# Kernel tuning notes

Measured on AMD Instinct MI355X. Metric: run time of the kernel, lower is better.

## Reference

```python
import jax, jax.numpy as jnp
import numpy as np

EPS = 1e-6
K_HOPS = 2  # SGConv K


def setup_inputs() -> dict:
    key = jax.random.key(0)
    k1, k2, k3, k4 = jax.random.split(key, 4)
    B, Kk, C, T = 32, 8, 64, 250
    E, H = 4096, 128
    x = jax.random.normal(k1, (B, Kk, C, T), dtype=jnp.float32)
    edge_index = jax.random.randint(k2, (2, E), 0, C, dtype=jnp.int64)
    edge_weights = jax.random.uniform(k3, (E,), dtype=jnp.float32)
    W = jax.random.normal(k4, (H, Kk * T), dtype=jnp.float32) * 0.02
    b = jnp.zeros((H,), dtype=jnp.float32)
    return {"x": x, "edge_index": edge_index, "edge_weights": edge_weights, "W": W, "b": b}


def reference(x, edge_index, edge_weights, W, b):
    B, Kk, C, T = x.shape
    N = C  # nodes
    x = x.reshape(B, N, Kk * T)  # (B, N, F)

    # clamp non-positive edge weights to epsilon (mirrors in-place .data clamp)
    w = jnp.where(edge_weights <= 0, EPS, edge_weights)

    # gcn_norm with self loops (fill value 1.0)
    src, dst = edge_index[0], edge_index[1]
    loop = jnp.arange(N, dtype=edge_index.dtype)
    src = jnp.concatenate([src, loop])
    dst = jnp.concatenate([dst, loop])
    w = jnp.concatenate([w, jnp.ones((N,), w.dtype)])
    deg = jnp.zeros((N,), w.dtype).at[dst].add(w)
    dinv = jnp.where(deg > 0, deg ** -0.5, jnp.zeros_like(deg))
    norm = dinv[src] * w * dinv[dst]  # (E+N,)

    # K hops of gather -> weight -> scatter-add aggregation
    for _ in range(K_HOPS):
        msg = x[:, src, :] * norm[None, :, None]        # (B, E+N, F)
        x = jnp.zeros_like(x).at[:, dst, :].add(msg)    # (B, N, F)

    # final linear: y = x @ W^T + b
    return jnp.einsum('bnf,hf->bnh', x, W) + b
```

## Files before the change

kernel.cpp:

```cpp
#include <hip/hip_runtime.h>
#include <hip/hip_bf16.h>

#define EPSW 1e-6f

typedef __attribute__((ext_vector_type(4))) float floatx4;
typedef __attribute__((ext_vector_type(4))) unsigned int uintx4;
typedef __attribute__((ext_vector_type(8))) short shortx8;

__device__ __forceinline__ unsigned short f2bf(float f) {
    unsigned int u = __float_as_uint(f);
    u = (u + 0x7fffu + ((u >> 16) & 1u)) >> 16;
    return (unsigned short)u;
}

__device__ __forceinline__ unsigned int pk2(float lo, float hi) {
    return (unsigned int)f2bf(lo) | ((unsigned int)f2bf(hi) << 16);
}

__device__ __forceinline__ uintx4 pk8(floatx4 a, floatx4 b) {
    uintx4 r;
    r.x = pk2(a.x, a.y); r.y = pk2(a.z, a.w);
    r.z = pk2(b.x, b.y); r.w = pk2(b.z, b.w);
    return r;
}

__global__ __launch_bounds__(256) void gemm_mt(
        const float* __restrict__ x,
        const float* __restrict__ W,
        const int* __restrict__ ei,
        const float* __restrict__ ew,
        float* __restrict__ zp,
        float* __restrict__ Mt) {
    __shared__ __align__(16) unsigned char smem[2][20480];
    const int bid = blockIdx.x;
    const int t   = threadIdx.x;

    if (bid >= 512) {
        const int bm = bid - 512;
        float* A    = (float*)smem;
        float* deg  = A + 4096;
        float* dinv = deg + 64;
        if (t < 64) deg[t] = 1.0f;
        for (int i = t; i < 4096; i += 256) A[i] = 0.0f;
        __syncthreads();
        const int* srcp = ei;
        const int* dstp = ei + 4096;
#pragma unroll
        for (int i = 0; i < 16; ++i) {
            const int e = i * 256 + t;
            float w = ew[e];
            w = (w <= 0.0f) ? EPSW : w;
            atomicAdd(&deg[dstp[e]], w);
        }
        __syncthreads();
        if (t < 64) dinv[t] = 1.0f / sqrtf(deg[t]);
        __syncthreads();
#pragma unroll
        for (int i = 0; i < 16; ++i) {
            const int e = i * 256 + t;
            float w = ew[e];
            w = (w <= 0.0f) ? EPSW : w;
            const int s = srcp[e], d = dstp[e];
            atomicAdd(&A[d * 64 + s], dinv[s] * w * dinv[d]);
        }
        if (t < 64) atomicAdd(&A[t * 64 + t], dinv[t] * dinv[t]);
        __syncthreads();
        const int c  = t & 63;
        const int rr = t >> 6;
        float s0 = 0.f, s1 = 0.f, s2 = 0.f, s3 = 0.f;
#pragma unroll 8
        for (int k = 0; k < 64; ++k) {
            const float akc = A[k * 64 + c];
            const float* an = A + (bm * 16 + rr * 4) * 64 + k;
            s0 += an[0]   * akc;
            s1 += an[64]  * akc;
            s2 += an[128] * akc;
            s3 += an[192] * akc;
        }
        float* mo = Mt + c * 64 + bm * 16 + rr * 4;
        mo[0] = s0; mo[1] = s1; mo[2] = s2; mo[3] = s3;
        return;
    }

    const int ks    = bid & 7;
    const int bb2   = bid >> 3;
    const int rbase = bb2 * 32;
    const int kbase = ks * 256;

    const int wave = t >> 6, lane = t & 63;
    const int m = lane & 15, q = lane >> 4;
    const int kq = t & 7;
    const int rw = t >> 3;

    floatx4 acc[2][2];
#pragma unroll
    for (int rt = 0; rt < 2; ++rt)
#pragma unroll
        for (int hh = 0; hh < 2; ++hh)
            acc[rt][hh] = (floatx4){0.f, 0.f, 0.f, 0.f};

    floatx4 rA[2][2];
    floatx4 rB[2][8];

#define LOADC(c)                                                              \
    {                                                                         \
        const int s_ = (c) & 1;                                               \
        const int k_ = kbase + (c) * 64 + kq * 8;                             \
        if (k_ < 2000) {                                                      \
            const float* pa_ = x + (size_t)(rbase + rw) * 2000 + k_;          \
            rA[s_][0] = *(const floatx4*)pa_;                                 \
            rA[s_][1] = *(const floatx4*)(pa_ + 4);                           \
            _Pragma("unroll")                                                 \
            for (int j_ = 0; j_ < 4; ++j_) {                                  \
                const float* pw_ = W + (size_t)(rw + 32 * j_) * 2000 + k_;    \
                rB[s_][j_ * 2]     = *(const floatx4*)pw_;                    \
                rB[s_][j_ * 2 + 1] = *(const floatx4*)(pw_ + 4);              \
            }                                                                 \
        } else {                                                              \
            rA[s_][0] = rA[s_][1] = (floatx4){0.f, 0.f, 0.f, 0.f};            \
            _Pragma("unroll")                                                 \
            for (int j_ = 0; j_ < 8; ++j_)                                    \
                rB[s_][j_] = (floatx4){0.f, 0.f, 0.f, 0.f};                   \
        }                                                                     \
    }

#define WRITEC(c)                                                             \
    {                                                                         \
        const int s_ = (c) & 1;                                               \
        unsigned char* sb_ = smem[s_];                                        \
        *(uintx4*)(sb_ + kq * 512 + rw * 16) = pk8(rA[s_][0], rA[s_][1]);     \
        _Pragma("unroll")                                                     \
        for (int j_ = 0; j_ < 4; ++j_)                                        \
            *(uintx4*)(sb_ + 4096 + kq * 2048 + (rw + 32 * j_) * 16) =        \
                pk8(rB[s_][j_ * 2], rB[s_][j_ * 2 + 1]);                      \
    }

    LOADC(0);
    LOADC(1);
#pragma unroll
    for (int c = 0; c < 4; ++c) {
        WRITEC(c);
        if (c < 2) LOADC(c + 2);
        __syncthreads();
        const unsigned char* sb = smem[c & 1];
#pragma unroll
        for (int p = 0; p < 2; ++p) {
            const int kgq = p * 4 + q;
            shortx8 af[2];
#pragma unroll
            for (int rt = 0; rt < 2; ++rt)
                af[rt] = *(const shortx8*)(sb + kgq * 512 + (rt * 16 + m) * 16);
            shortx8 bf[2];
#pragma unroll
            for (int hh = 0; hh < 2; ++hh)
                bf[hh] = *(const shortx8*)(sb + 4096 + kgq * 2048 +
                                           ((wave + hh * 4) * 16 + m) * 16);
#pragma unroll
            for (int rt = 0; rt < 2; ++rt)
#pragma unroll
                for (int hh = 0; hh < 2; ++hh)
                    acc[rt][hh] = __builtin_amdgcn_mfma_f32_16x16x32_bf16(
                        af[rt], bf[hh], acc[rt][hh], 0, 0, 0);
        }
    }
#undef LOADC
#undef WRITEC

    float* zslice = zp + ((size_t)ks * 2048 + rbase) * 128;
#pragma unroll
    for (int rt = 0; rt < 2; ++rt)
#pragma unroll
        for (int hh = 0; hh < 2; ++hh) {
            const int h = (wave + hh * 4) * 16 + m;
#pragma unroll
            for (int v = 0; v < 4; ++v) {
                const int n = rt * 16 + q * 4 + v;
                zslice[n * 128 + h] = acc[rt][hh][v];
            }
        }
}

__global__ __launch_bounds__(256) void apply_M(const float* __restrict__ zp,
                                               const float* __restrict__ Mtg,
                                               const float* __restrict__ bias,
                                               float* __restrict__ y) {
    __shared__ float Ms[4096];
    __shared__ float zs[64][16];
    const int b  = blockIdx.x;
    const int hc = blockIdx.y;
    const int t  = threadIdx.x;
#pragma unroll
    for (int i = 0; i < 16; ++i) Ms[i * 256 + t] = Mtg[i * 256 + t];
#pragma unroll
    for (int i = 0; i < 4; ++i) {
        const int idx = i * 256 + t;
        const int mr = idx >> 4, hh = idx & 15;
        float s = 0.0f;
#pragma unroll
        for (int ks = 0; ks < 8; ++ks)
            s += zp[((size_t)ks * 2048 + b * 64 + mr) * 128 + hc * 16 + hh];
        zs[mr][hh] = s;
    }
    __syncthreads();
    const int h  = t & 15;
    const int n0 = (t >> 4) * 4;
    const float bv = bias[hc * 16 + h];
    float s0 = bv, s1 = bv, s2 = bv, s3 = bv;
#pragma unroll
    for (int mm = 0; mm < 64; ++mm) {
        const float zv = zs[mm][h];
        s0 += Ms[mm * 64 + n0 + 0] * zv;
        s1 += Ms[mm * 64 + n0 + 1] * zv;
        s2 += Ms[mm * 64 + n0 + 2] * zv;
        s3 += Ms[mm * 64 + n0 + 3] * zv;
    }
    float* yp = y + (size_t)b * 8192 + (size_t)n0 * 128 + hc * 16 + h;
    yp[0]   = s0;
    yp[128] = s1;
    yp[256] = s2;
    yp[384] = s3;
}

extern "C" void kernel_launch(void* const* d_in, const int* in_sizes, int n_in,
                              void* d_out, int out_size, void* d_ws, size_t ws_size,
                              hipStream_t stream) {
    const float* x    = (const float*)d_in[0];
    const int*   ei   = (const int*)d_in[1];
    const float* ew   = (const float*)d_in[2];
    const float* W    = (const float*)d_in[3];
    const float* bias = (const float*)d_in[4];
    float* y = (float*)d_out;

    float* zp = (float*)d_ws;
    float* Mt = zp + 2097152;

    gemm_mt<<<516, 256, 0, stream>>>(x, W, ei, ew, zp, Mt);
    apply_M<<<dim3(32, 8), 256, 0, stream>>>(zp, Mt, bias, y);
}
```

Measured before the change: 93.57 us.

## Load MFMA fragments directly from global memory and double the row tile

The GEMM stops staging tiles through shared memory. Each lane now loads its own bf16 MFMA fragments straight from global memory into registers and prefetches the next chunk one step ahead, so the LDS writes, reads and barriers go away. The row tile doubles to 64, which halves the GEMM grid to 256 blocks and lets each wave reuse its W fragments over four row tiles. In exchange, every wave reloads the same W and x data from global memory or L2 instead of sharing it, register pressure rises, and fewer blocks are available to spread across the CUs.

Result: no change. 94.42 us (+0.9%).

```diff
diff --git a/kernel.cpp b/kernel.cpp
--- a/kernel.cpp
+++ b/kernel.cpp
@@ -17,11 +17,11 @@
     return (unsigned int)f2bf(lo) | ((unsigned int)f2bf(hi) << 16);
 }
 
-__device__ __forceinline__ uintx4 pk8(floatx4 a, floatx4 b) {
-    uintx4 r;
-    r.x = pk2(a.x, a.y); r.y = pk2(a.z, a.w);
-    r.z = pk2(b.x, b.y); r.w = pk2(b.z, b.w);
-    return r;
+__device__ __forceinline__ shortx8 pk8s(floatx4 a, floatx4 b) {
+    union { uintx4 u; shortx8 s; } r;
+    r.u.x = pk2(a.x, a.y); r.u.y = pk2(a.z, a.w);
+    r.u.z = pk2(b.x, b.y); r.u.w = pk2(b.z, b.w);
+    return r.s;
 }
 
 __global__ __launch_bounds__(256) void gemm_mt(
@@ -31,13 +31,13 @@
         const float* __restrict__ ew,
         float* __restrict__ zp,
         float* __restrict__ Mt) {
-    __shared__ __align__(16) unsigned char smem[2][20480];
+    __shared__ float sA[4224];
     const int bid = blockIdx.x;
     const int t   = threadIdx.x;
 
-    if (bid >= 512) {
-        const int bm = bid - 512;
-        float* A    = (float*)smem;
+    if (bid >= 256) {
+        const int bm = bid - 256;
+        float* A    = sA;
         float* deg  = A + 4096;
         float* dinv = deg + 64;
         if (t < 64) deg[t] = 1.0f;
@@ -83,92 +83,89 @@
     }
 
     const int ks    = bid & 7;
-    const int bb2   = bid >> 3;
-    const int rbase = bb2 * 32;
+    const int rtile = bid >> 3;
+    const int rbase = rtile * 64;
     const int kbase = ks * 256;
 
     const int wave = t >> 6, lane = t & 63;
     const int m = lane & 15, q = lane >> 4;
-    const int kq = t & 7;
-    const int rw = t >> 3;
-
-    floatx4 acc[2][2];
-#pragma unroll
-    for (int rt = 0; rt < 2; ++rt)
+
+    const float* xr[4];
+    const float* wr[2];
+#pragma unroll
+    for (int rt = 0; rt < 4; ++rt)
+        xr[rt] = x + (size_t)(rbase + rt * 16 + m) * 2000;
+#pragma unroll
+    for (int hh = 0; hh < 2; ++hh)
+        wr[hh] = W + (size_t)((wave + hh * 4) * 16 + m) * 2000;
+
+    floatx4 acc[4][2];
+#pragma unroll
+    for (int rt = 0; rt < 4; ++rt)
 #pragma unroll
         for (int hh = 0; hh < 2; ++hh)
             acc[rt][hh] = (floatx4){0.f, 0.f, 0.f, 0.f};
 
-    floatx4 rA[2][2];
-    floatx4 rB[2][8];
+    floatx4 fx[4][2][2];
+    floatx4 fw[2][2][2];
 
 #define LOADC(c)                                                              \
     {                                                                         \
-        const int s_ = (c) & 1;                                               \
-        const int k_ = kbase + (c) * 64 + kq * 8;                             \
-        if (k_ < 2000) {                                                      \
-            const float* pa_ = x + (size_t)(rbase + rw) * 2000 + k_;          \
-            rA[s_][0] = *(const floatx4*)pa_;                                 \
-            rA[s_][1] = *(const floatx4*)(pa_ + 4);                           \
-            _Pragma("unroll")                                                 \
-            for (int j_ = 0; j_ < 4; ++j_) {                                  \
-                const float* pw_ = W + (size_t)(rw + 32 * j_) * 2000 + k_;    \
-                rB[s_][j_ * 2]     = *(const floatx4*)pw_;                    \
-                rB[s_][j_ * 2 + 1] = *(const floatx4*)(pw_ + 4);              \
+        _Pragma("unroll")                                                     \
+        for (int p_ = 0; p_ < 2; ++p_) {                                      \
+            const int k_ = kbase + (c) * 64 + (p_ * 4 + q) * 8;               \
+            if (k_ < 2000) {                                                  \
+                _Pragma("unroll")                                             \
+                for (int rt_ = 0; rt_ < 4; ++rt_) {                           \
+                    fx[rt_][p_][0] = *(const floatx4*)(xr[rt_] + k_);         \
+                    fx[rt_][p_][1] = *(const floatx4*)(xr[rt_] + k_ + 4);     \
+                }                                                             \
+                _Pragma("unroll")                                             \
+                for (int hh_ = 0; hh_ < 2; ++hh_) {                           \
+                    fw[hh_][p_][0] = *(const floatx4*)(wr[hh_] + k_);         \
+                    fw[hh_][p_][1] = *(const floatx4*)(wr[hh_] + k_ + 4);     \
+                }                                                             \
+            } else {                                                          \
+                _Pragma("unroll")                                             \
+                for (int rt_ = 0; rt_ < 4; ++rt_)                             \
+                    fx[rt_][p_][0] = fx[rt_][p_][1] =                         \
+                        (floatx4){0.f, 0.f, 0.f, 0.f};                        \
+                _Pragma("unroll")                                             \
+                for (int hh_ = 0; hh_ < 2; ++hh_)                             \
+                    fw[hh_][p_][0] = fw[hh_][p_][1] =                         \
+                        (floatx4){0.f, 0.f, 0.f, 0.f};                        \
             }                                                                 \
-        } else {                                                              \
-            rA[s_][0] = rA[s_][1] = (floatx4){0.f, 0.f, 0.f, 0.f};            \
-            _Pragma("unroll")                                                 \
-            for (int j_ = 0; j_ < 8; ++j_)                                    \
-                rB[s_][j_] = (floatx4){0.f, 0.f, 0.f, 0.f};                   \
         }                                                                     \
     }
 
-#define WRITEC(c)                                                             \
-    {                                                                         \
-        const int s_ = (c) & 1;                                               \
-        unsigned char* sb_ = smem[s_];                                        \
-        *(uintx4*)(sb_ + kq * 512 + rw * 16) = pk8(rA[s_][0], rA[s_][1]);     \
-        _Pragma("unroll")                                                     \
-        for (int j_ = 0; j_ < 4; ++j_)                                        \
-            *(uintx4*)(sb_ + 4096 + kq * 2048 + (rw + 32 * j_) * 16) =        \
-                pk8(rB[s_][j_ * 2], rB[s_][j_ * 2 + 1]);                      \
-    }
-
     LOADC(0);
-    LOADC(1);
 #pragma unroll
     for (int c = 0; c < 4; ++c) {
-        WRITEC(c);
-        if (c < 2) LOADC(c + 2);
-        __syncthreads();
-        const unsigned char* sb = smem[c & 1];
+        shortx8 af[4][2], bf[2][2];
 #pragma unroll
         for (int p = 0; p < 2; ++p) {
-            const int kgq = p * 4 + q;
-            shortx8 af[2];
-#pragma unroll
-            for (int rt = 0; rt < 2; ++rt)
-                af[rt] = *(const shortx8*)(sb + kgq * 512 + (rt * 16 + m) * 16);
-            shortx8 bf[2];
+#pragma unroll
+            for (int rt = 0; rt < 4; ++rt)
+                af[rt][p] = pk8s(fx[rt][p][0], fx[rt][p][1]);
 #pragma unroll
             for (int hh = 0; hh < 2; ++hh)
-                bf[hh] = *(const shortx8*)(sb + 4096 + kgq * 2048 +
-                                           ((wave + hh * 4) * 16 + m) * 16);
-#pragma unroll
-            for (int rt = 0; rt < 2; ++rt)
+                bf[hh][p] = pk8s(fw[hh][p][0], fw[hh][p][1]);
+        }
+        if (c < 3) LOADC(c + 1);
+#pragma unroll
+        for (int p = 0; p < 2; ++p)
+#pragma unroll
+            for (int rt = 0; rt < 4; ++rt)
 #pragma unroll
                 for (int hh = 0; hh < 2; ++hh)
                     acc[rt][hh] = __builtin_amdgcn_mfma_f32_16x16x32_bf16(
-                        af[rt], bf[hh], acc[rt][hh], 0, 0, 0);
-        }
+                        af[rt][p], bf[hh][p], acc[rt][hh], 0, 0, 0);
     }
 #undef LOADC
-#undef WRITEC
 
     float* zslice = zp + ((size_t)ks * 2048 + rbase) * 128;
 #pragma unroll
-    for (int rt = 0; rt < 2; ++rt)
+    for (int rt = 0; rt < 4; ++rt)
 #pragma unroll
         for (int hh = 0; hh < 2; ++hh) {
             const int h = (wave + hh * 4) * 16 + m;
@@ -234,6 +231,6 @@
     float* zp = (float*)d_ws;
     float* Mt = zp + 2097152;
 
-    gemm_mt<<<516, 256, 0, stream>>>(x, W, ei, ew, zp, Mt);
+    gemm_mt<<<260, 256, 0, stream>>>(x, W, ei, ew, zp, Mt);
     apply_M<<<dim3(32, 8), 256, 0, stream>>>(zp, Mt, bias, y);
 }
```
